# Performance work log

Measured on AMD Instinct MI355X. Metric: run time of the kernel, lower is better.

Reference implementation:

```python
import jax, jax.numpy as jnp
import numpy as np

FUZZY_FACTOR = 2
REG_WT = 0.0008


def setup_inputs() -> dict:
    key = jax.random.key(0)
    k1, k2 = jax.random.split(key)
    logits = jax.random.normal(k1, (2, 4, 128, 128, 128), dtype=jnp.float32)
    y_pred = jax.nn.softmax(logits, axis=1)  # module assumes softmax already applied
    image = jax.random.normal(k2, (2, 1, 128, 128, 128), dtype=jnp.float32)
    return {"y_pred": y_pred, "image": image}


def _neighbor_sum(x):
    # x: [B, K, D, H, W]; 3x3x3 ones kernel with zero center, SAME padding,
    # applied independently per (batch, cluster) channel.
    B, K, D, H, W = x.shape
    kernel = jnp.ones((1, 1, 3, 3, 3), x.dtype).at[0, 0, 1, 1, 1].set(0.0)
    y = jax.lax.conv_general_dilated(
        x.reshape(B * K, 1, D, H, W), kernel,
        window_strides=(1, 1, 1), padding="SAME",
        dimension_numbers=("NCDHW", "OIDHW", "NCDHW"))
    return y.reshape(B, K, D, H, W)


def reference(y_pred, image):
    B, K = y_pred.shape[0], y_pred.shape[1]
    N = int(np.prod(y_pred.shape[2:]))
    pred = y_pred.reshape(B, K, N)          # [B, K, N]
    img = image.reshape(B, N)               # [B, N]

    mem = pred ** FUZZY_FACTOR              # fuzzy memberships [B, K, N]

    # cluster centroids v_k = sum(img*mem)/sum(mem)  -> [B, K]
    v = jnp.sum(img[:, None, :] * mem, axis=2) / jnp.sum(mem, axis=2)

    # J_1 = sum_i mem_i * (img - v_i)^2   -> [B, N]
    J1 = jnp.sum(mem * (img[:, None, :] - v[:, :, None]) ** 2, axis=1)

    # neighbor sum of each cluster's membership map (box filter minus center)
    nb = _neighbor_sum(mem.reshape(y_pred.shape)).reshape(B, K, N)
    # sum over j != i, computed once as total - self (identical algebra)
    J_in = jnp.sum(nb, axis=1, keepdims=True) - nb  # [B, K, N]
    J2 = jnp.sum(mem * J_in, axis=1)                # [B, N]

    return jnp.mean(J1) + REG_WT * jnp.mean(J2)
```

## Files before the change

### kernel.cpp

```cpp
#include <hip/hip_runtime.h>


#define BB 2
#define KK 4
#define DD 128
#define HH 128
#define WW 128
#define PLANE (HH * WW)
#define SD 4
#define NBD (DD / SD)
#define HR 8
#define NBH (HH / HR)
#define NT 256

__global__ __launch_bounds__(NT) void rfcm_main(
    const float* __restrict__ yp, const float* __restrict__ img,
    double* __restrict__ ws)
{
    __shared__ double red[4 * 13];

    const int tid = threadIdx.x;
    const int wv  = tid >> 6;
    const int L   = tid & 63;
    const int wl  = L & 31;
    const int hy  = L >> 5;
    const int c0  = wl << 2;

    const int bid  = blockIdx.x;
    const int xcd  = bid & 7;
    const int idx  = bid >> 3;
    const int sl   = idx >> 4;
    const int ht   = idx & 15;
    const int slab = sl * 8 + xcd;
    const int b    = slab >> 5;
    const int dsb  = slab & 31;

    const int h0  = ht * HR;
    const int hp0 = h0 + (wv << 1);
    const int h   = hp0 + hy;
    const int d0  = dsb * SD;

    const int gHr = (hy == 0) ? (hp0 - 1) : (hp0 + 2);
    const int gH  = gHr < 0 ? 0 : (gHr > HH - 1 ? HH - 1 : gHr);
    const float hsc = (gHr >= 0 && gHr <= HH - 1) ? 1.f : 0.f;

    const bool okL = (wl > 0), okR = (wl < 31);

    const float* pO[KK];
    const long dH = (long)(gH - h) * WW;
    #pragma unroll
    for (int k = 0; k < KK; k++)
        pO[k] = yp + (size_t)((b * KK + k) * DD) * PLANE + (size_t)h * WW + c0;

    float4 oA[KK], aA[KK], oB[KK], aB[KK];

    auto lplane = [&](int t, float4* o, float4* a) {
        const size_t off = (size_t)t * PLANE;
        #pragma unroll
        for (int k = 0; k < KK; k++) {
            o[k] = *(const float4*)(pO[k] + off);
            a[k] = *(const float4*)(pO[k] + off + dH);
        }
    };

    auto extract = [&](const float4 o4, const float4 a4, float4& s9, float4& mm) {
        const float4 m = make_float4(o4.x*o4.x, o4.y*o4.y, o4.z*o4.z, o4.w*o4.w);
        mm = m;
        float4 p;
        p.x = __shfl_xor(m.x, 32, 64);
        p.y = __shfl_xor(m.y, 32, 64);
        p.z = __shfl_xor(m.z, 32, 64);
        p.w = __shfl_xor(m.w, 32, 64);
        float4 v;
        v.x = fmaf(a4.x*a4.x, hsc, m.x + p.x);
        v.y = fmaf(a4.y*a4.y, hsc, m.y + p.y);
        v.z = fmaf(a4.z*a4.z, hsc, m.z + p.z);
        v.w = fmaf(a4.w*a4.w, hsc, m.w + p.w);
        const float vL = okL ? __shfl_up(v.w, 1)   : 0.f;
        const float vR = okR ? __shfl_down(v.x, 1) : 0.f;
        s9.x = vL  + v.x + v.y;
        s9.y = v.x + v.y + v.z;
        s9.z = v.y + v.z + v.w;
        s9.w = v.z + v.w + vR;
    };

    const float* imgb = img + (size_t)b * DD * PLANE + (size_t)h * WW + c0;

    const bool vprev = (d0 > 0);
    lplane(vprev ? d0 - 1 : 0, oA, aA);
    lplane(d0, oB, aB);
    float4 iv = *(const float4*)(imgb + (size_t)d0 * PLANE);

    float4 s9p[KK], s9c[KK], mc[KK], dum;
    #pragma unroll
    for (int k = 0; k < KK; k++) extract(oA[k], aA[k], s9p[k], dum);
    if (!vprev) {
        #pragma unroll
        for (int k = 0; k < KK; k++) s9p[k] = make_float4(0.f, 0.f, 0.f, 0.f);
    }
    lplane(d0 + 1, oA, aA);
    #pragma unroll
    for (int k = 0; k < KK; k++) extract(oB[k], aB[k], s9c[k], mc[k]);

    float smf[KK] = {0,0,0,0}, sif[KK] = {0,0,0,0}, saf[KK] = {0,0,0,0};
    float j2f = 0.f;

    auto step = [&](int i, float4* oC, float4* aC, float4* oP, float4* aP) {
        const int d = d0 + i;
        const bool vn = (d + 1 < DD);
        float4 ivn = iv;
        if (vn) ivn = *(const float4*)(imgb + (size_t)(d + 1) * PLANE);
        if (i < SD - 1 && d + 2 < DD) lplane(d + 2, oP, aP);

        const float4 iv2 = make_float4(iv.x*iv.x, iv.y*iv.y, iv.z*iv.z, iv.w*iv.w);
        float4 summ  = make_float4(0.f, 0.f, 0.f, 0.f);
        float4 sumbk = make_float4(0.f, 0.f, 0.f, 0.f);
        float4 cross = make_float4(0.f, 0.f, 0.f, 0.f);

        #pragma unroll
        for (int k = 0; k < KK; k++) {
            float4 s9n, mn;
            if (vn) extract(oC[k], aC[k], s9n, mn);
            else { s9n = make_float4(0.f,0.f,0.f,0.f); mn = s9n; }

            const float4 m = mc[k];
            float4 bk;
            bk.x = s9p[k].x + s9c[k].x + s9n.x;
            bk.y = s9p[k].y + s9c[k].y + s9n.y;
            bk.z = s9p[k].z + s9c[k].z + s9n.z;
            bk.w = s9p[k].w + s9c[k].w + s9n.w;

            summ.x += m.x; summ.y += m.y; summ.z += m.z; summ.w += m.w;
            sumbk.x += bk.x; sumbk.y += bk.y; sumbk.z += bk.z; sumbk.w += bk.w;
            cross.x = fmaf(m.x, bk.x - m.x, cross.x);
            cross.y = fmaf(m.y, bk.y - m.y, cross.y);
            cross.z = fmaf(m.z, bk.z - m.z, cross.z);
            cross.w = fmaf(m.w, bk.w - m.w, cross.w);

            smf[k] += (m.x + m.y) + (m.z + m.w);
            sif[k] = fmaf(m.x, iv.x,  fmaf(m.y, iv.y,  fmaf(m.z, iv.z,  fmaf(m.w, iv.w,  sif[k]))));
            saf[k] = fmaf(m.x, iv2.x, fmaf(m.y, iv2.y, fmaf(m.z, iv2.z, fmaf(m.w, iv2.w, saf[k]))));

            s9p[k] = s9c[k]; s9c[k] = s9n; mc[k] = mn;
        }

        j2f += (summ.x * (sumbk.x - summ.x) - cross.x)
             + (summ.y * (sumbk.y - summ.y) - cross.y)
             + (summ.z * (sumbk.z - summ.z) - cross.z)
             + (summ.w * (sumbk.w - summ.w) - cross.w);

        iv = ivn;
    };

    #pragma unroll
    for (int ii = 0; ii < SD / 2; ii++) {
        step(2 * ii,     oA, aA, oB, aB);
        step(2 * ii + 1, oB, aB, oA, aA);
    }

    double q[13];
    #pragma unroll
    for (int k = 0; k < KK; k++) {
        q[k] = (double)smf[k]; q[4 + k] = (double)sif[k]; q[8 + k] = (double)saf[k];
    }
    q[12] = (double)j2f;

    #pragma unroll
    for (int qq = 0; qq < 13; qq++) {
        double v = q[qq];
        #pragma unroll
        for (int off = 32; off > 0; off >>= 1) v += __shfl_down(v, off, 64);
        q[qq] = v;
    }

    const int lane = tid & 63, wid = tid >> 6;
    if (lane == 0) {
        #pragma unroll
        for (int qq = 0; qq < 13; qq++) red[wid * 13 + qq] = q[qq];
    }
    __syncthreads();
    if (tid < 13) {
        const double sfin = red[tid] + red[13 + tid] + red[26 + tid] + red[39 + tid];
        int idxo;
        if      (tid < 4)  idxo = b * KK + tid;
        else if (tid < 8)  idxo = 8  + b * KK + (tid - 4);
        else if (tid < 12) idxo = 16 + b * KK + (tid - 8);
        else               idxo = 24;
        unsafeAtomicAdd(&ws[idxo], sfin);
    }
}

__global__ void rfcm_fin(const double* __restrict__ ws, float* __restrict__ out)
{
    if (threadIdx.x == 0 && blockIdx.x == 0) {
        double j1 = 0;
        #pragma unroll
        for (int i = 0; i < BB * KK; i++)
            j1 += ws[16 + i] - ws[8 + i] * ws[8 + i] / ws[i];
        const double invBN = 1.0 / ((double)BB * (double)DD * (double)HH * (double)WW);
        out[0] = (float)(j1 * invBN + 0.0008 * ws[24] * invBN);
    }
}

extern "C" void kernel_launch(void* const* d_in, const int* in_sizes, int n_in,
                              void* d_out, int out_size, void* d_ws, size_t ws_size,
                              hipStream_t stream) {
    const float* yp  = (const float*)d_in[0];
    const float* img = (const float*)d_in[1];
    float* out = (float*)d_out;
    double* ws = (double*)d_ws;

    hipMemsetAsync(d_ws, 0, 25 * sizeof(double), stream);

    dim3 grid(BB * NBD * NBH);
    rfcm_main<<<grid, NT, 0, stream>>>(yp, img, ws);
    rfcm_fin<<<1, 64, 0, stream>>>(ws, out);
}
```

Baseline: 134.3 us.

## Restructure J2 neighbor sum with per-plane algebraic decomposition and deeper depth slabs

Each wave now owns one full row (float2 per lane) and loads the up, center and down rows directly, replacing the cross-half shuffle scheme. The J2 cross term is rewritten so that each plane's membership is multiplied against the previous, current and next plane's 9-point sums through per-plane totals (M, S, Mp, Sp), which avoids building the full 27-point box sum per cluster. The depth slab grows from 4 to 8 planes, which reduces the redundant halo-plane loads, and the block now covers 4 rows instead of 8. The trade-offs are three loads per plane per cluster, narrower float2 accesses, and a more involved boundary handling at the end of each slab.

```diff
diff --git a/kernel.cpp b/kernel.cpp
--- a/kernel.cpp
+++ b/kernel.cpp
@@ -7,10 +7,10 @@
 #define HH 128
 #define WW 128
 #define PLANE (HH * WW)
-#define SD 4
+#define SD 8
 #define NBD (DD / SD)
-#define HR 8
-#define NBH (HH / HR)
+#define HRB 4
+#define NBH (HH / HRB)
 #define NT 256
 
 __global__ __launch_bounds__(NT) void rfcm_main(
@@ -22,161 +22,164 @@
     const int tid = threadIdx.x;
     const int wv  = tid >> 6;
     const int L   = tid & 63;
-    const int wl  = L & 31;
-    const int hy  = L >> 5;
-    const int c0  = wl << 2;
+    const int c0  = L << 1;
 
     const int bid  = blockIdx.x;
     const int xcd  = bid & 7;
     const int idx  = bid >> 3;
-    const int sl   = idx >> 4;
-    const int ht   = idx & 15;
+    const int sl   = idx >> 5;
+    const int ht   = idx & 31;
     const int slab = sl * 8 + xcd;
-    const int b    = slab >> 5;
-    const int dsb  = slab & 31;
-
-    const int h0  = ht * HR;
-    const int hp0 = h0 + (wv << 1);
-    const int h   = hp0 + hy;
-    const int d0  = dsb * SD;
-
-    const int gHr = (hy == 0) ? (hp0 - 1) : (hp0 + 2);
-    const int gH  = gHr < 0 ? 0 : (gHr > HH - 1 ? HH - 1 : gHr);
-    const float hsc = (gHr >= 0 && gHr <= HH - 1) ? 1.f : 0.f;
-
-    const bool okL = (wl > 0), okR = (wl < 31);
-
-    const float* pO[KK];
-    const long dH = (long)(gH - h) * WW;
+    const int b    = slab >> 4;
+    const int dsb  = slab & 15;
+
+    const int h  = ht * HRB + wv;
+    const int d0 = dsb * SD;
+
+    const float su = (h > 0)      ? 1.f : 0.f;
+    const float sd = (h < HH - 1) ? 1.f : 0.f;
+    const int   oU = (h > 0)      ? -WW : 0;
+    const int   oD = (h < HH - 1) ?  WW : 0;
+
+    const bool okL = (L > 0), okR = (L < 63);
+
+    const float* pk[KK];
     #pragma unroll
     for (int k = 0; k < KK; k++)
-        pO[k] = yp + (size_t)((b * KK + k) * DD) * PLANE + (size_t)h * WW + c0;
-
-    float4 oA[KK], aA[KK], oB[KK], aB[KK];
-
-    auto lplane = [&](int t, float4* o, float4* a) {
+        pk[k] = yp + (size_t)((b * KK + k) * DD) * PLANE + (size_t)h * WW + c0;
+    const float* imgb = img + (size_t)b * DD * PLANE + (size_t)h * WW + c0;
+
+    float2 uA[KK], oA[KK], dA[KK], uB[KK], oB[KK], dB[KK];
+
+    auto lplane = [&](int t, float2* u, float2* o, float2* d) {
         const size_t off = (size_t)t * PLANE;
         #pragma unroll
         for (int k = 0; k < KK; k++) {
-            o[k] = *(const float4*)(pO[k] + off);
-            a[k] = *(const float4*)(pO[k] + off + dH);
+            const float* p = pk[k] + off;
+            u[k] = *(const float2*)(p + oU);
+            o[k] = *(const float2*)(p);
+            d[k] = *(const float2*)(p + oD);
         }
     };
 
-    auto extract = [&](const float4 o4, const float4 a4, float4& s9, float4& mm) {
-        const float4 m = make_float4(o4.x*o4.x, o4.y*o4.y, o4.z*o4.z, o4.w*o4.w);
-        mm = m;
-        float4 p;
-        p.x = __shfl_xor(m.x, 32, 64);
-        p.y = __shfl_xor(m.y, 32, 64);
-        p.z = __shfl_xor(m.z, 32, 64);
-        p.w = __shfl_xor(m.w, 32, 64);
-        float4 v;
-        v.x = fmaf(a4.x*a4.x, hsc, m.x + p.x);
-        v.y = fmaf(a4.y*a4.y, hsc, m.y + p.y);
-        v.z = fmaf(a4.z*a4.z, hsc, m.z + p.z);
-        v.w = fmaf(a4.w*a4.w, hsc, m.w + p.w);
-        const float vL = okL ? __shfl_up(v.w, 1)   : 0.f;
-        const float vR = okR ? __shfl_down(v.x, 1) : 0.f;
-        s9.x = vL  + v.x + v.y;
-        s9.y = v.x + v.y + v.z;
-        s9.z = v.y + v.z + v.w;
-        s9.w = v.z + v.w + vR;
+    auto extract = [&](const float2 u, const float2 o, const float2 dn,
+                       float2& m, float2& s9) {
+        m.x = o.x * o.x; m.y = o.y * o.y;
+        float2 v;
+        v.x = fmaf(u.x * u.x, su, fmaf(dn.x * dn.x, sd, m.x));
+        v.y = fmaf(u.y * u.y, su, fmaf(dn.y * dn.y, sd, m.y));
+        const float vl = okL ? __shfl_up(v.y, 1)   : 0.f;
+        const float vr = okR ? __shfl_down(v.x, 1) : 0.f;
+        s9.x = vl + v.x + v.y;
+        s9.y = v.x + v.y + vr;
     };
 
-    const float* imgb = img + (size_t)b * DD * PLANE + (size_t)h * WW + c0;
-
-    const bool vprev = (d0 > 0);
-    lplane(vprev ? d0 - 1 : 0, oA, aA);
-    lplane(d0, oB, aB);
-    float4 iv = *(const float4*)(imgb + (size_t)d0 * PLANE);
-
-    float4 s9p[KK], s9c[KK], mc[KK], dum;
-    #pragma unroll
-    for (int k = 0; k < KK; k++) extract(oA[k], aA[k], s9p[k], dum);
-    if (!vprev) {
-        #pragma unroll
-        for (int k = 0; k < KK; k++) s9p[k] = make_float4(0.f, 0.f, 0.f, 0.f);
-    }
-    lplane(d0 + 1, oA, aA);
-    #pragma unroll
-    for (int k = 0; k < KK; k++) extract(oB[k], aB[k], s9c[k], mc[k]);
+    const int tp = (d0 > 0) ? d0 - 1 : d0;
+    lplane(tp, uA, oA, dA);
+    lplane(d0, uB, oB, dB);
+    float2 iv = *(const float2*)(imgb + (size_t)d0 * PLANE);
+
+    float2 mp[KK], sp[KK];
+    float2 Mp, Sp; Mp.x = Mp.y = Sp.x = Sp.y = 0.f;
+    #pragma unroll
+    for (int k = 0; k < KK; k++) {
+        float2 m, s9;
+        extract(uA[k], oA[k], dA[k], m, s9);
+        mp[k] = m; sp[k] = s9;
+        Mp.x += m.x; Mp.y += m.y; Sp.x += s9.x; Sp.y += s9.y;
+    }
+    if (d0 == 0) {
+        #pragma unroll
+        for (int k = 0; k < KK; k++) {
+            mp[k].x = mp[k].y = 0.f; sp[k].x = sp[k].y = 0.f;
+        }
+        Mp.x = Mp.y = Sp.x = Sp.y = 0.f;
+    }
+    lplane(d0 + 1, uA, oA, dA);
 
     float smf[KK] = {0,0,0,0}, sif[KK] = {0,0,0,0}, saf[KK] = {0,0,0,0};
     float j2f = 0.f;
 
-    auto step = [&](int i, float4* oC, float4* aC, float4* oP, float4* aP) {
-        const int d = d0 + i;
-        const bool vn = (d + 1 < DD);
-        float4 ivn = iv;
-        if (vn) ivn = *(const float4*)(imgb + (size_t)(d + 1) * PLANE);
-        if (i < SD - 1 && d + 2 < DD) lplane(d + 2, oP, aP);
-
-        const float4 iv2 = make_float4(iv.x*iv.x, iv.y*iv.y, iv.z*iv.z, iv.w*iv.w);
-        float4 summ  = make_float4(0.f, 0.f, 0.f, 0.f);
-        float4 sumbk = make_float4(0.f, 0.f, 0.f, 0.f);
-        float4 cross = make_float4(0.f, 0.f, 0.f, 0.f);
-
-        #pragma unroll
-        for (int k = 0; k < KK; k++) {
-            float4 s9n, mn;
-            if (vn) extract(oC[k], aC[k], s9n, mn);
-            else { s9n = make_float4(0.f,0.f,0.f,0.f); mn = s9n; }
-
-            const float4 m = mc[k];
-            float4 bk;
-            bk.x = s9p[k].x + s9c[k].x + s9n.x;
-            bk.y = s9p[k].y + s9c[k].y + s9n.y;
-            bk.z = s9p[k].z + s9c[k].z + s9n.z;
-            bk.w = s9p[k].w + s9c[k].w + s9n.w;
-
-            summ.x += m.x; summ.y += m.y; summ.z += m.z; summ.w += m.w;
-            sumbk.x += bk.x; sumbk.y += bk.y; sumbk.z += bk.z; sumbk.w += bk.w;
-            cross.x = fmaf(m.x, bk.x - m.x, cross.x);
-            cross.y = fmaf(m.y, bk.y - m.y, cross.y);
-            cross.z = fmaf(m.z, bk.z - m.z, cross.z);
-            cross.w = fmaf(m.w, bk.w - m.w, cross.w);
-
-            smf[k] += (m.x + m.y) + (m.z + m.w);
-            sif[k] = fmaf(m.x, iv.x,  fmaf(m.y, iv.y,  fmaf(m.z, iv.z,  fmaf(m.w, iv.w,  sif[k]))));
-            saf[k] = fmaf(m.x, iv2.x, fmaf(m.y, iv2.y, fmaf(m.z, iv2.z, fmaf(m.w, iv2.w, saf[k]))));
-
-            s9p[k] = s9c[k]; s9c[k] = s9n; mc[k] = mn;
-        }
-
-        j2f += (summ.x * (sumbk.x - summ.x) - cross.x)
-             + (summ.y * (sumbk.y - summ.y) - cross.y)
-             + (summ.z * (sumbk.z - summ.z) - cross.z)
-             + (summ.w * (sumbk.w - summ.w) - cross.w);
-
+    auto step = [&](int i, float2* uC, float2* oC, float2* dC) {
+        const int t = d0 + i;
+        float2 ivn = iv;
+        if (i < SD - 1) ivn = *(const float2*)(imgb + (size_t)(t + 1) * PLANE);
+        const bool reload = (i < SD - 2) || (i == SD - 2 && d0 + SD < DD);
+        const size_t off2 = (size_t)(t + 2) * PLANE;
+
+        const float ivx2 = iv.x * iv.x, ivy2 = iv.y * iv.y;
+        float2 M, S; M.x = M.y = S.x = S.y = 0.f;
+        float q = 0.f, ctt = 0.f, ctp = 0.f, cpt = 0.f;
+
+        #pragma unroll
+        for (int k = 0; k < KK; k++) {
+            float2 m, s9;
+            extract(uC[k], oC[k], dC[k], m, s9);
+            if (reload) {
+                const float* p = pk[k] + off2;
+                uC[k] = *(const float2*)(p + oU);
+                oC[k] = *(const float2*)(p);
+                dC[k] = *(const float2*)(p + oD);
+            }
+            M.x += m.x; M.y += m.y; S.x += s9.x; S.y += s9.y;
+            q   = fmaf(m.x, m.x,      fmaf(m.y, m.y,      q));
+            ctt = fmaf(m.x, s9.x,     fmaf(m.y, s9.y,     ctt));
+            ctp = fmaf(m.x, sp[k].x,  fmaf(m.y, sp[k].y,  ctp));
+            if (i > 0)
+                cpt = fmaf(mp[k].x, s9.x, fmaf(mp[k].y, s9.y, cpt));
+            smf[k] += m.x + m.y;
+            sif[k] = fmaf(m.x, iv.x, fmaf(m.y, iv.y, sif[k]));
+            saf[k] = fmaf(m.x, ivx2, fmaf(m.y, ivy2, saf[k]));
+            mp[k] = m; sp[k] = s9;
+        }
+
+        j2f += (M.x * S.x + M.y * S.y) - (M.x * M.x + M.y * M.y) + q - ctt
+             + (M.x * Sp.x + M.y * Sp.y) - ctp;
+        if (i > 0)
+            j2f += (Mp.x * S.x + Mp.y * S.y) - cpt;
+
+        Mp = M; Sp = S;
         iv = ivn;
     };
 
     #pragma unroll
     for (int ii = 0; ii < SD / 2; ii++) {
-        step(2 * ii,     oA, aA, oB, aB);
-        step(2 * ii + 1, oB, aB, oA, aA);
-    }
-
-    double q[13];
+        step(2 * ii,     uB, oB, dB);
+        step(2 * ii + 1, uA, oA, dA);
+    }
+
+    if (d0 + SD < DD) {
+        float2 S; S.x = S.y = 0.f;
+        float cpt = 0.f;
+        #pragma unroll
+        for (int k = 0; k < KK; k++) {
+            float2 m, s9;
+            extract(uB[k], oB[k], dB[k], m, s9);
+            S.x += s9.x; S.y += s9.y;
+            cpt = fmaf(mp[k].x, s9.x, fmaf(mp[k].y, s9.y, cpt));
+        }
+        j2f += (Mp.x * S.x + Mp.y * S.y) - cpt;
+    }
+
+    double qd[13];
     #pragma unroll
     for (int k = 0; k < KK; k++) {
-        q[k] = (double)smf[k]; q[4 + k] = (double)sif[k]; q[8 + k] = (double)saf[k];
-    }
-    q[12] = (double)j2f;
+        qd[k] = (double)smf[k]; qd[4 + k] = (double)sif[k]; qd[8 + k] = (double)saf[k];
+    }
+    qd[12] = (double)j2f;
 
     #pragma unroll
     for (int qq = 0; qq < 13; qq++) {
-        double v = q[qq];
+        double v = qd[qq];
         #pragma unroll
         for (int off = 32; off > 0; off >>= 1) v += __shfl_down(v, off, 64);
-        q[qq] = v;
+        qd[qq] = v;
     }
 
     const int lane = tid & 63, wid = tid >> 6;
     if (lane == 0) {
         #pragma unroll
-        for (int qq = 0; qq < 13; qq++) red[wid * 13 + qq] = q[qq];
+        for (int qq = 0; qq < 13; qq++) red[wid * 13 + qq] = qd[qq];
     }
     __syncthreads();
     if (tid < 13) {
```

Result: no change. 132.5 us (-1.3%).
